# Kernel optimization log

Hardware: AMD Instinct MI355X
Metric: run time of the kernel (lower is better)

Reference implementation:

```python
import jax, jax.numpy as jnp
import numpy as np

B, L = 4, 2048
D_MODEL, D_INNER, D_STATE, DT_RANK, K = 512, 1024, 16, 64, 4


def setup_inputs() -> dict:
    key = jax.random.key(0)
    ks = jax.random.split(key, 21)
    def n(k, shape, s=0.02):
        return (jax.random.normal(k, shape) * s).astype(jnp.float32)
    inp = {"x": jax.random.normal(ks[0], (B, L, D_MODEL), jnp.float32)}
    for i, sfx in enumerate(("f", "b")):
        o = 1 + i * 8
        inp[f"W_in_{sfx}"] = n(ks[o], (2 * D_INNER, D_MODEL))
        inp[f"conv_w_{sfx}"] = n(ks[o + 1], (D_INNER, 1, K), 0.1)
        inp[f"conv_b_{sfx}"] = jnp.zeros((D_INNER,), jnp.float32)
        inp[f"A_log_{sfx}"] = (jax.random.normal(ks[o + 2], (D_STATE, D_INNER)) * 0.1).astype(jnp.float32)
        inp[f"D_{sfx}"] = jnp.ones((D_INNER,), jnp.float32)
        inp[f"Wx_{sfx}"] = n(ks[o + 3], (DT_RANK + 2 * D_STATE, D_INNER))
        inp[f"Wdt_{sfx}"] = n(ks[o + 4], (D_INNER, DT_RANK), DT_RANK ** -0.5)
        dt = jnp.exp(jax.random.uniform(ks[o + 5], (D_INNER,)) * (np.log(0.1) - np.log(0.001)) + np.log(0.001))
        inp[f"bdt_{sfx}"] = (dt + jnp.log(-jnp.expm1(-dt))).astype(jnp.float32)
        inp[f"Wout_{sfx}"] = n(ks[o + 6], (D_MODEL, D_INNER))
    return inp


def _mamba_block(x, W_in, conv_w, conv_b, A_log, Dp, Wx, Wdt, bdt, Wout):
    # x: [B, L, d_model]
    xz = jnp.einsum('bld,ed->ble', x, W_in)              # [B, L, 2*d_inner]
    xb, zb = xz[..., :D_INNER], xz[..., D_INNER:]
    # causal depthwise conv over time
    xc = jnp.transpose(xb, (0, 2, 1))                     # [B, M, L]
    xc = jax.lax.conv_general_dilated(
        xc, conv_w, window_strides=(1,), padding=[(K - 1, 0)],
        feature_group_count=D_INNER,
        dimension_numbers=('NCH', 'OIH', 'NCH')) + conv_b[None, :, None]
    xb = jax.nn.silu(jnp.transpose(xc, (0, 2, 1)))        # [B, L, M]
    # input-dependent SSM parameters
    proj = jnp.einsum('blm,pm->blp', xb, Wx)              # [B, L, dt_rank+2D]
    dt_in = proj[..., :DT_RANK]
    Bs = proj[..., DT_RANK:DT_RANK + D_STATE]             # [B, L, D]
    Cs = proj[..., DT_RANK + D_STATE:]                    # [B, L, D]
    dt = jax.nn.softplus(jnp.einsum('blr,mr->blm', dt_in, Wdt) + bdt)  # [B, L, M]
    A_T = -jnp.exp(A_log).T                               # [M, D]

    def step(h, inp):
        dt_t, x_t, B_t, C_t = inp                         # [B,M],[B,M],[B,D],[B,D]
        dA = jnp.exp(dt_t[:, :, None] * A_T[None])        # [B, M, D]
        h = dA * h + (dt_t * x_t)[:, :, None] * B_t[:, None, :]
        y_t = jnp.einsum('bmd,bd->bm', h, C_t)
        return h, y_t

    xs = (jnp.moveaxis(dt, 1, 0), jnp.moveaxis(xb, 1, 0),
          jnp.moveaxis(Bs, 1, 0), jnp.moveaxis(Cs, 1, 0))
    h0 = jnp.zeros((x.shape[0], D_INNER, D_STATE), x.dtype)
    _, ys = jax.lax.scan(step, h0, xs)                    # [L, B, M]
    y = jnp.moveaxis(ys, 0, 1) + Dp * xb                  # [B, L, M]
    y = y * jax.nn.silu(zb)                               # SiLU gate
    return jnp.einsum('blm,dm->bld', y, Wout)             # [B, L, d_model]


def reference(x,
              W_in_f, conv_w_f, conv_b_f, A_log_f, D_f, Wx_f, Wdt_f, bdt_f, Wout_f,
              W_in_b, conv_w_b, conv_b_b, A_log_b, D_b, Wx_b, Wdt_b, bdt_b, Wout_b):
    out_f = _mamba_block(x, W_in_f, conv_w_f, conv_b_f, A_log_f, D_f, Wx_f, Wdt_f, bdt_f, Wout_f)
    out_b = jnp.flip(_mamba_block(jnp.flip(x, 1), W_in_b, conv_w_b, conv_b_b, A_log_b, D_b, Wx_b, Wdt_b, bdt_b, Wout_b), 1)
    return out_f + out_b
```

## Files before the change

kernel.cpp:

```cpp
#include <hip/hip_runtime.h>
#include <hip/hip_bf16.h>
#include <cstdint>
#include <cstdio>

typedef float f32x4 __attribute__((ext_vector_type(4)));
typedef short s16x8 __attribute__((ext_vector_type(8)));

__device__ __forceinline__ float us2f(unsigned short u){
  union { unsigned int i; float f; } v; v.i = ((unsigned int)u) << 16; return v.f;
}
__device__ __forceinline__ unsigned short f2us(float f){
  union { float f; unsigned int i; } v; v.f = f;
  unsigned int r = v.i + 0x7fffu + ((v.i >> 16) & 1u);
  return (unsigned short)(r >> 16);
}
__device__ __forceinline__ s16x8 pack_bf8(f32x4 lo, f32x4 hi){
  s16x8 r;
  r[0]=(short)f2us(lo[0]); r[1]=(short)f2us(lo[1]); r[2]=(short)f2us(lo[2]); r[3]=(short)f2us(lo[3]);
  r[4]=(short)f2us(hi[0]); r[5]=(short)f2us(hi[1]); r[6]=(short)f2us(hi[2]); r[7]=(short)f2us(hi[3]);
  return r;
}

__global__ __launch_bounds__(256)
void prep_k(const float* __restrict__ x,
            const float* __restrict__ W_in_f, const float* __restrict__ W_in_b,
            const float* __restrict__ Wx_f,   const float* __restrict__ Wx_b,
            const float* __restrict__ Wdt_f,  const float* __restrict__ Wdt_b,
            const float* __restrict__ Wout_f, const float* __restrict__ Wout_b,
            const float* __restrict__ Alog_f, const float* __restrict__ Alog_b,
            const float* __restrict__ bdt_f,  const float* __restrict__ bdt_b,
            unsigned short* __restrict__ W1cat, unsigned short* __restrict__ Wxpad,
            unsigned short* __restrict__ Wdtb,  unsigned short* __restrict__ Woutcat,
            float* __restrict__ A2, float* __restrict__ bdtcat,
            unsigned short* __restrict__ xbf)
{
  long i = (long)blockIdx.x * 256 + threadIdx.x;
  if (i < 4194304) {
    xbf[i] = f2us(x[i]); return;
  }
  i -= 4194304;
  if (i < 2097152) {
    int n = (int)(i >> 9), k = (int)(i & 511);
    float v = (n < 2048) ? W_in_f[(long)n*512 + k] : W_in_b[(long)(n-2048)*512 + k];
    W1cat[i] = f2us(v); return;
  }
  i -= 2097152;
  if (i < 262144) {
    int dir = (int)(i >> 17); long r = i & 131071; int n = (int)(r >> 10), k = (int)(r & 1023);
    const float* Wx = dir ? Wx_b : Wx_f;
    Wxpad[(long)dir*131072 + r] = f2us(n < 96 ? Wx[(long)n*1024 + k] : 0.f); return;
  }
  i -= 262144;
  if (i < 131072) {
    int dir = (int)(i >> 16); long r = i & 65535;
    Wdtb[i] = f2us((dir ? Wdt_b : Wdt_f)[r]); return;
  }
  i -= 131072;
  if (i < 1048576) {
    int n = (int)(i >> 11), k = (int)(i & 2047);
    float v = (k < 1024) ? Wout_f[(long)n*1024 + k] : Wout_b[(long)n*1024 + (k-1024)];
    Woutcat[i] = f2us(v); return;
  }
  i -= 1048576;
  if (i < 32768) {
    int dir = (int)(i >> 14); long r = i & 16383; int m = (int)(r >> 4), d = (int)(r & 15);
    const float* Al = dir ? Alog_b : Alog_f;
    A2[i] = -__expf(Al[(long)d*1024 + m]) * 1.4426950408889634f; return;
  }
  i -= 32768;
  if (i < 2048) {
    int dir = (int)(i >> 10), m = (int)(i & 1023);
    bdtcat[i] = (dir ? bdt_b : bdt_f)[m]; return;
  }
}

template<int OUT_MODE, int A_IS_F32>
__global__ __launch_bounds__(256)
void gemm_bt(const void* __restrict__ Ap, const unsigned short* __restrict__ Bp,
             void* __restrict__ Cp, const float* __restrict__ biasp,
             int K, int lda, int ldb, int ldc,
             long az, long bz, long cz, int biasz)
{
  const int z   = blockIdx.z;
  const int tid = threadIdx.x;
  const int bm  = blockIdx.x, bn = blockIdx.y;

  __shared__ __align__(16) unsigned short Ash[128][32];
  __shared__ __align__(16) unsigned short Bsh[128][32];

  const int wave = tid >> 6, lane = tid & 63;
  const int wr = (wave >> 1) << 6, wc = (wave & 1) << 6;
  const int fr = lane & 15, fs = lane >> 4;

  const int r0 = tid >> 2, r1 = r0 + 64;
  const int sg = tid & 3,  kofs = sg << 3;

  const unsigned short* A16 = (const unsigned short*)Ap + (long)z * az;
  const float*          A32 = (const float*)Ap          + (long)z * az;
  const unsigned short* Bg  = Bp + (long)z * bz;

  const long aoff0 = (long)(bm*128 + r0)*lda + kofs;
  const long aoff1 = (long)(bm*128 + r1)*lda + kofs;
  const long boff0 = (long)(bn*128 + r0)*ldb + kofs;
  const long boff1 = (long)(bn*128 + r1)*ldb + kofs;

  f32x4 acc[4][4];
  #pragma unroll
  for (int i=0;i<4;i++)
    #pragma unroll
    for (int j=0;j<4;j++) acc[i][j] = (f32x4){0.f,0.f,0.f,0.f};

  s16x8 a0r{}, a1r{}, b0r{}, b1r{};
  f32x4 alo0{}, ahi0{}, alo1{}, ahi1{};

  if (A_IS_F32){
    alo0 = *(const f32x4*)(A32 + aoff0); ahi0 = *(const f32x4*)(A32 + aoff0 + 4);
    alo1 = *(const f32x4*)(A32 + aoff1); ahi1 = *(const f32x4*)(A32 + aoff1 + 4);
  } else {
    a0r = *(const s16x8*)(A16 + aoff0);
    a1r = *(const s16x8*)(A16 + aoff1);
  }
  b0r = *(const s16x8*)(Bg + boff0);
  b1r = *(const s16x8*)(Bg + boff1);

  const int NK  = K >> 5;
  const int sw0 = (sg ^ ((r0 >> 1) & 3)) << 3;
  const int sw1 = (sg ^ ((r1 >> 1) & 3)) << 3;

  for (int ks = 0; ks < NK; ++ks){
    __syncthreads();
    if (A_IS_F32){
      *(s16x8*)&Ash[r0][sw0] = pack_bf8(alo0, ahi0);
      *(s16x8*)&Ash[r1][sw1] = pack_bf8(alo1, ahi1);
    } else {
      *(s16x8*)&Ash[r0][sw0] = a0r;
      *(s16x8*)&Ash[r1][sw1] = a1r;
    }
    *(s16x8*)&Bsh[r0][sw0] = b0r;
    *(s16x8*)&Bsh[r1][sw1] = b1r;
    __syncthreads();
    if (ks + 1 < NK){
      const long k0 = (long)(ks + 1) << 5;
      if (A_IS_F32){
        alo0 = *(const f32x4*)(A32 + aoff0 + k0); ahi0 = *(const f32x4*)(A32 + aoff0 + k0 + 4);
        alo1 = *(const f32x4*)(A32 + aoff1 + k0); ahi1 = *(const f32x4*)(A32 + aoff1 + k0 + 4);
      } else {
        a0r = *(const s16x8*)(A16 + aoff0 + k0);
        a1r = *(const s16x8*)(A16 + aoff1 + k0);
      }
      b0r = *(const s16x8*)(Bg + boff0 + k0);
      b1r = *(const s16x8*)(Bg + boff1 + k0);
    }
    s16x8 af[4], bfv[4];
    #pragma unroll
    for (int i=0;i<4;i++){
      const int ar = wr + i*16 + fr;
      af[i]  = *(const s16x8*)&Ash[ar][(fs ^ ((ar >> 1) & 3)) << 3];
      const int br = wc + i*16 + fr;
      bfv[i] = *(const s16x8*)&Bsh[br][(fs ^ ((br >> 1) & 3)) << 3];
    }
    #pragma unroll
    for (int i=0;i<4;i++)
      #pragma unroll
      for (int j=0;j<4;j++)
        acc[i][j] = __builtin_amdgcn_mfma_f32_16x16x32_bf16(af[i], bfv[j], acc[i][j], 0, 0, 0);
  }

  #pragma unroll
  for (int i=0;i<4;i++){
    const int rowb = bm*128 + wr + i*16 + (fs << 2);
    #pragma unroll
    for (int j=0;j<4;j++){
      const int col = bn*128 + wc + j*16 + fr;
      #pragma unroll
      for (int e=0;e<4;e++){
        float v = acc[i][j][e];
        const long cidx = (long)z*cz + (long)(rowb + e)*ldc + col;
        if (OUT_MODE == 2){
          ((float*)Cp)[cidx] = v;
        } else if (OUT_MODE == 1){
          v += biasp[z*biasz + col];
          v = fmaxf(v, 0.f) + log1pf(__expf(-fabsf(v)));
          ((unsigned short*)Cp)[cidx] = f2us(v);
        } else {
          ((unsigned short*)Cp)[cidx] = f2us(v);
        }
      }
    }
  }
}

__global__ __launch_bounds__(256)
void conv_silu_k(const unsigned short* __restrict__ xz,
                 const float* __restrict__ wf, const float* __restrict__ cbf,
                 const float* __restrict__ wb, const float* __restrict__ cbb,
                 unsigned short* __restrict__ xbc)
{
  const long idx = (long)blockIdx.x * 256 + threadIdx.x;
  const int  col = (int)(idx & 2047);
  const long tok = idx >> 11;
  const int  dir = col >> 10, m = col & 1023;
  const int  l   = (int)(tok & 2047);
  const long rowb = tok << 12;
  const float* w  = dir ? wb : wf;
  float acc = dir ? cbb[m] : cbf[m];
  const int xcol = (dir << 11) + m;
  #pragma unroll
  for (int k=0;k<4;k++){
    const int pos = dir ? (l + 3 - k) : (l - 3 + k);
    if (pos >= 0 && pos < 2048)
      acc += w[m*4 + k] * us2f(xz[rowb + ((long)(pos - l) << 12) + xcol]);
  }
  const float s = acc / (1.f + __expf(-acc));
  xbc[idx] = f2us(s);
}

#define SCHUNK 64
#define NCHUNK 32

__global__ __launch_bounds__(256)
void scan1_k(const unsigned short* __restrict__ dtb, const unsigned short* __restrict__ xbc,
             const unsigned short* __restrict__ proj, const float* __restrict__ A2,
             float* __restrict__ hloc, float* __restrict__ Ssum)
{
  const int tidx = threadIdx.x;
  const int cb = blockIdx.x, c = blockIdx.y, bz = blockIdx.z;
  const int b = bz >> 1, dir = bz & 1;
  const int m = cb*256 + tidx;

  float a2[16];
  { const f32x4* p = (const f32x4*)(A2 + (((long)dir*1024 + m) << 4));
    f32x4 v0=p[0], v1=p[1], v2=p[2], v3=p[3];
    #pragma unroll
    for (int e=0;e<4;e++){ a2[e]=v0[e]; a2[4+e]=v1[e]; a2[8+e]=v2[e]; a2[12+e]=v3[e]; } }

  __shared__ float Bs[SCHUNK][16];
  if (tidx < 128){
    const int t = tidx >> 1, half = tidx & 1;
    const int l = dir ? (2047 - (c*SCHUNK + t)) : (c*SCHUNK + t);
    const long tok = (long)b*2048 + l;
    const s16x8 v = *(const s16x8*)(proj + (long)dir*1048576 + tok*128 + 64 + half*8);
    #pragma unroll
    for (int e=0;e<8;e++) Bs[t][half*8 + e] = us2f((unsigned short)v[e]);
  }
  __syncthreads();

  const int  l0 = dir ? (2047 - c*SCHUNK) : (c*SCHUNK);
  const int  ls = dir ? -1 : 1;
  const long tok0 = (long)b*2048 + l0;
  const unsigned short* dtp = dtb + (((long)dir) << 23) + tok0*1024 + m;
  const unsigned short* xvp = xbc + tok0*2048 + (dir << 10) + m;
  const long dstp = (long)ls*1024, xstp = (long)ls*2048;

  float h[16];
  #pragma unroll
  for (int d=0;d<16;d++) h[d]=0.f;
  float S = 0.f;

  unsigned short du = *dtp, xu = *xvp;
  for (int t=0;t<SCHUNK;t++){
    const float dt = us2f(du), xv = us2f(xu);
    dtp += dstp; xvp += xstp;
    du = *dtp; xu = *xvp;
    S += dt;
    const float u = dt * xv;
    const f32x4* bp = (const f32x4*)&Bs[t][0];
    f32x4 bv0=bp[0], bv1=bp[1], bv2=bp[2], bv3=bp[3];
    #pragma unroll
    for (int d=0;d<16;d++){
      const float bval = (d<4)? bv0[d&3] : (d<8)? bv1[d&3] : (d<12)? bv2[d&3] : bv3[d&3];
      const float a = __builtin_amdgcn_exp2f(dt * a2[d]);
      h[d] = __builtin_fmaf(a, h[d], u * bval);
    }
  }
  const long o = ((((long)bz * NCHUNK) + c)*1024 + m);
  f32x4* Hp = (f32x4*)(hloc + (o << 4));
  #pragma unroll
  for (int q=0;q<4;q++){
    f32x4 hv;
    #pragma unroll
    for (int e=0;e<4;e++) hv[e]=h[q*4+e];
    Hp[q]=hv;
  }
  Ssum[o] = S;
}

__global__ __launch_bounds__(256)
void scan2_k(const float* __restrict__ A2, const float* __restrict__ Ssum,
             float* __restrict__ hloc)
{
  const long idx = (long)blockIdx.x*256 + threadIdx.x;
  const long bz = idx >> 14; const int r = (int)(idx & 16383);
  const int dir = (int)(bz & 1);
  const float a2 = A2[((long)dir << 14) + r];
  const long base = bz * NCHUNK;
  float hs = 0.f;
  float hlN = hloc[base*16384 + r];
  float SN  = Ssum[base*1024 + (r >> 4)];
  for (int c=0;c<NCHUNK;c++){
    const float hl = hlN, Sv = SN;
    const int cn = (c+1 < NCHUNK) ? c+1 : c;
    hlN = hloc[(base+cn)*16384 + r];
    SN  = Ssum[(base+cn)*1024 + (r >> 4)];
    const float P = __builtin_amdgcn_exp2f(a2 * Sv);
    hloc[(base+c)*16384 + r] = hs;
    hs = __builtin_fmaf(P, hs, hl);
  }
}

__global__ __launch_bounds__(256)
void scan3_k(const unsigned short* __restrict__ dtb, const unsigned short* __restrict__ xbc,
             const unsigned short* __restrict__ proj, const float* __restrict__ A2,
             const float* __restrict__ hstart, const unsigned short* __restrict__ xz,
             const float* __restrict__ D_f, const float* __restrict__ D_b,
             unsigned short* __restrict__ ybuf)
{
  const int tidx = threadIdx.x;
  const int cb = blockIdx.x, c = blockIdx.y, bz = blockIdx.z;
  const int b = bz >> 1, dir = bz & 1;
  const int m = cb*256 + tidx;

  float a2[16];
  { const f32x4* p = (const f32x4*)(A2 + (((long)dir*1024 + m) << 4));
    f32x4 v0=p[0], v1=p[1], v2=p[2], v3=p[3];
    #pragma unroll
    for (int e=0;e<4;e++){ a2[e]=v0[e]; a2[4+e]=v1[e]; a2[8+e]=v2[e]; a2[12+e]=v3[e]; } }
  const float Dm = (dir ? D_b : D_f)[m];

  __shared__ float Bs[SCHUNK][16];
  __shared__ float Cs[SCHUNK][16];
  {
    const int half = tidx & 1;
    if (tidx < 128){
      const int t = tidx >> 1;
      const int l = dir ? (2047 - (c*SCHUNK + t)) : (c*SCHUNK + t);
      const long tok = (long)b*2048 + l;
      const s16x8 vb = *(const s16x8*)(proj + (long)dir*1048576 + tok*128 + 64 + half*8);
      #pragma unroll
      for (int e=0;e<8;e++) Bs[t][half*8+e] = us2f((unsigned short)vb[e]);
    } else {
      const int t = (tidx - 128) >> 1;
      const int l = dir ? (2047 - (c*SCHUNK + t)) : (c*SCHUNK + t);
      const long tok = (long)b*2048 + l;
      const s16x8 vc = *(const s16x8*)(proj + (long)dir*1048576 + tok*128 + 80 + half*8);
      #pragma unroll
      for (int e=0;e<8;e++) Cs[t][half*8+e] = us2f((unsigned short)vc[e]);
    }
  }

  float h[16];
  { const long o = ((((long)bz*NCHUNK) + c)*1024 + m) << 4;
    const f32x4* p = (const f32x4*)(hstart + o);
    f32x4 v0=p[0], v1=p[1], v2=p[2], v3=p[3];
    #pragma unroll
    for (int e=0;e<4;e++){ h[e]=v0[e]; h[4+e]=v1[e]; h[8+e]=v2[e]; h[12+e]=v3[e]; } }
  __syncthreads();

  const int  l0 = dir ? (2047 - c*SCHUNK) : (c*SCHUNK);
  const int  ls = dir ? -1 : 1;
  const long tok0 = (long)b*2048 + l0;
  const unsigned short* dtp = dtb + (((long)dir) << 23) + tok0*1024 + m;
  const unsigned short* xvp = xbc + tok0*2048 + (dir << 10) + m;
  const unsigned short* zp  = xz  + (tok0 << 12) + (dir << 11) + 1024 + m;
  unsigned short*       yp  = ybuf + tok0*2048 + (dir << 10) + m;
  const long dstp = (long)ls*1024, xstp = (long)ls*2048, zstp = (long)ls << 12;

  unsigned short du = *dtp, xu = *xvp, zu = *zp;
  for (int t=0;t<SCHUNK;t++){
    const float dt = us2f(du), xv = us2f(xu), zb = us2f(zu);
    dtp += dstp; xvp += xstp; zp += zstp;
    du = *dtp; xu = *xvp; zu = *zp;
    const float u = dt * xv;
    const f32x4* bp = (const f32x4*)&Bs[t][0];
    const f32x4* cp = (const f32x4*)&Cs[t][0];
    f32x4 bv0=bp[0], bv1=bp[1], bv2=bp[2], bv3=bp[3];
    f32x4 cv0=cp[0], cv1=cp[1], cv2=cp[2], cv3=cp[3];
    float y0=0.f, y1=0.f, y2=0.f, y3=0.f;
    #pragma unroll
    for (int d=0;d<16;d++){
      const float bval = (d<4)? bv0[d&3] : (d<8)? bv1[d&3] : (d<12)? bv2[d&3] : bv3[d&3];
      const float cval = (d<4)? cv0[d&3] : (d<8)? cv1[d&3] : (d<12)? cv2[d&3] : cv3[d&3];
      const float a = __builtin_amdgcn_exp2f(dt * a2[d]);
      h[d] = __builtin_fmaf(a, h[d], u * bval);
      if (d<4)       y0 = __builtin_fmaf(h[d], cval, y0);
      else if (d<8)  y1 = __builtin_fmaf(h[d], cval, y1);
      else if (d<12) y2 = __builtin_fmaf(h[d], cval, y2);
      else           y3 = __builtin_fmaf(h[d], cval, y3);
    }
    float y = ((y0+y1)+(y2+y3)) + Dm * xv;
    const float gate = zb / (1.f + __expf(-zb));
    *yp = f2us(y * gate);
    yp += xstp;
  }
}

extern "C" void kernel_launch(void* const* d_in, const int* in_sizes, int n_in,
                              void* d_out, int out_size, void* d_ws, size_t ws_size,
                              hipStream_t stream)
{
  const float* x      = (const float*)d_in[0];
  const float* W_in_f = (const float*)d_in[1];
  const float* convw_f= (const float*)d_in[2];
  const float* convb_f= (const float*)d_in[3];
  const float* Alog_f = (const float*)d_in[4];
  const float* D_f    = (const float*)d_in[5];
  const float* Wx_f   = (const float*)d_in[6];
  const float* Wdt_f  = (const float*)d_in[7];
  const float* bdt_f  = (const float*)d_in[8];
  const float* Wout_f = (const float*)d_in[9];
  const float* W_in_b = (const float*)d_in[10];
  const float* convw_b= (const float*)d_in[11];
  const float* convb_b= (const float*)d_in[12];
  const float* Alog_b = (const float*)d_in[13];
  const float* D_b    = (const float*)d_in[14];
  const float* Wx_b   = (const float*)d_in[15];
  const float* Wdt_b  = (const float*)d_in[16];
  const float* bdt_b  = (const float*)d_in[17];
  const float* Wout_b = (const float*)d_in[18];

  char* w = (char*)d_ws;
  auto carve = [&](size_t bytes) -> char* {
    char* p = w; w += (bytes + 255) & ~(size_t)255; return p;
  };
  unsigned short* W1cat   = (unsigned short*)carve(4096ULL*512*2);
  unsigned short* Wxpad   = (unsigned short*)carve(2ULL*128*1024*2);
  unsigned short* Wdtb    = (unsigned short*)carve(2ULL*1024*64*2);
  unsigned short* Woutcat = (unsigned short*)carve(512ULL*2048*2);
  float*          A2      = (float*)carve(2ULL*1024*16*4);
  float*          bdtcat  = (float*)carve(2048ULL*4);
  unsigned short* xz      = (unsigned short*)carve(8192ULL*4096*2);
  unsigned short* xbc     = (unsigned short*)carve(8192ULL*2048*2);
  unsigned short* proj    = (unsigned short*)carve(2ULL*8192*128*2);
  unsigned short* dtb     = (unsigned short*)carve(2ULL*8192*1024*2);
  unsigned short* ybuf    = (unsigned short*)carve(8192ULL*2048*2);
  float*          hloc    = (float*)carve(8ULL*NCHUNK*1024*16*4);
  float*          Ssum    = (float*)carve(8ULL*NCHUNK*1024*4);
  unsigned short* xbf     = ybuf;

  if ((size_t)(w - (char*)d_ws) > ws_size) {
    fprintf(stderr, "kernel_launch: ws too small (%zu needed, %zu given)\n",
            (size_t)(w - (char*)d_ws), ws_size);
    return;
  }

  prep_k<<<dim3(30344), 256, 0, stream>>>(x, W_in_f, W_in_b, Wx_f, Wx_b, Wdt_f, Wdt_b,
                                          Wout_f, Wout_b, Alog_f, Alog_b, bdt_f, bdt_b,
                                          W1cat, Wxpad, Wdtb, Woutcat, A2, bdtcat, xbf);
  gemm_bt<0,0><<<dim3(64,32,1), 256, 0, stream>>>(xbf, W1cat, xz, nullptr,
                                                  512, 512, 512, 4096, 0, 0, 0, 0);
  conv_silu_k<<<dim3(65536), 256, 0, stream>>>(xz, convw_f, convb_f, convw_b, convb_b, xbc);
  gemm_bt<0,0><<<dim3(64,1,2), 256, 0, stream>>>(xbc, Wxpad, proj, nullptr,
                                                 1024, 2048, 1024, 128,
                                                 1024, 131072, 1048576, 0);
  gemm_bt<1,0><<<dim3(64,8,2), 256, 0, stream>>>(proj, Wdtb, dtb, bdtcat,
                                                 64, 128, 64, 1024,
                                                 1048576, 65536, 8388608, 1024);
  scan1_k<<<dim3(4,NCHUNK,8), 256, 0, stream>>>(dtb, xbc, proj, A2, hloc, Ssum);
  scan2_k<<<dim3(512), 256, 0, stream>>>(A2, Ssum, hloc);
  scan3_k<<<dim3(4,NCHUNK,8), 256, 0, stream>>>(dtb, xbc, proj, A2, hloc, xz, D_f, D_b, ybuf);
  gemm_bt<2,0><<<dim3(64,4,1), 256, 0, stream>>>(ybuf, Woutcat, d_out, nullptr,
                                                 2048, 2048, 2048, 512, 0, 0, 0, 0);
}
```

Measured before the change: 355.8 us.

## Use direct global-to-LDS loads in GEMM and vectorize conv+SiLU kernel

The GEMM now stages A and B tiles through global_load_lds (direct global-to-LDS DMA), replacing the register-prefetch path and the XOR swizzle. It also drops the unused fp32-A variant. The conv_silu kernel now processes 8 channels per thread with 16-byte vector loads and stores instead of one scalar per thread. The trade-off is that the GEMM loses its software prefetch overlap, since loads and compute are serialized around the barriers. Dropping the swizzle may also bring back LDS bank conflicts on the fragment reads.

```diff
diff --git a/kernel.cpp b/kernel.cpp
--- a/kernel.cpp
+++ b/kernel.cpp
@@ -14,11 +14,10 @@
   unsigned int r = v.i + 0x7fffu + ((v.i >> 16) & 1u);
   return (unsigned short)(r >> 16);
 }
-__device__ __forceinline__ s16x8 pack_bf8(f32x4 lo, f32x4 hi){
-  s16x8 r;
-  r[0]=(short)f2us(lo[0]); r[1]=(short)f2us(lo[1]); r[2]=(short)f2us(lo[2]); r[3]=(short)f2us(lo[3]);
-  r[4]=(short)f2us(hi[0]); r[5]=(short)f2us(hi[1]); r[6]=(short)f2us(hi[2]); r[7]=(short)f2us(hi[3]);
-  return r;
+__device__ __forceinline__ void gload_lds16(const void* g, void* l){
+  __builtin_amdgcn_global_load_lds(
+      (const __attribute__((address_space(1))) unsigned int*)g,
+      (__attribute__((address_space(3))) unsigned int*)l, 16, 0, 0);
 }
 
 __global__ __launch_bounds__(256)
@@ -74,9 +73,9 @@
   }
 }
 
-template<int OUT_MODE, int A_IS_F32>
-__global__ __launch_bounds__(256)
-void gemm_bt(const void* __restrict__ Ap, const unsigned short* __restrict__ Bp,
+template<int OUT_MODE>
+__global__ __launch_bounds__(256)
+void gemm_bt(const unsigned short* __restrict__ Ap, const unsigned short* __restrict__ Bp,
              void* __restrict__ Cp, const float* __restrict__ biasp,
              int K, int lda, int ldb, int ldc,
              long az, long bz, long cz, int biasz)
@@ -92,17 +91,21 @@
   const int wr = (wave >> 1) << 6, wc = (wave & 1) << 6;
   const int fr = lane & 15, fs = lane >> 4;
 
-  const int r0 = tid >> 2, r1 = r0 + 64;
-  const int sg = tid & 3,  kofs = sg << 3;
-
-  const unsigned short* A16 = (const unsigned short*)Ap + (long)z * az;
-  const float*          A32 = (const float*)Ap          + (long)z * az;
-  const unsigned short* Bg  = Bp + (long)z * bz;
+  const int r0 = tid >> 2;
+  const int sg = tid & 3, kofs = sg << 3;
+
+  const unsigned short* Ag = Ap + (long)z * az;
+  const unsigned short* Bg = Bp + (long)z * bz;
 
   const long aoff0 = (long)(bm*128 + r0)*lda + kofs;
-  const long aoff1 = (long)(bm*128 + r1)*lda + kofs;
+  const long aoff1 = aoff0 + (long)64*lda;
   const long boff0 = (long)(bn*128 + r0)*ldb + kofs;
-  const long boff1 = (long)(bn*128 + r1)*ldb + kofs;
+  const long boff1 = boff0 + (long)64*ldb;
+
+  unsigned short* lA0 = &Ash[r0][kofs];
+  unsigned short* lA1 = &Ash[64 + r0][kofs];
+  unsigned short* lB0 = &Bsh[r0][kofs];
+  unsigned short* lB1 = &Bsh[64 + r0][kofs];
 
   f32x4 acc[4][4];
   #pragma unroll
@@ -110,54 +113,21 @@
     #pragma unroll
     for (int j=0;j<4;j++) acc[i][j] = (f32x4){0.f,0.f,0.f,0.f};
 
-  s16x8 a0r{}, a1r{}, b0r{}, b1r{};
-  f32x4 alo0{}, ahi0{}, alo1{}, ahi1{};
-
-  if (A_IS_F32){
-    alo0 = *(const f32x4*)(A32 + aoff0); ahi0 = *(const f32x4*)(A32 + aoff0 + 4);
-    alo1 = *(const f32x4*)(A32 + aoff1); ahi1 = *(const f32x4*)(A32 + aoff1 + 4);
-  } else {
-    a0r = *(const s16x8*)(A16 + aoff0);
-    a1r = *(const s16x8*)(A16 + aoff1);
-  }
-  b0r = *(const s16x8*)(Bg + boff0);
-  b1r = *(const s16x8*)(Bg + boff1);
-
-  const int NK  = K >> 5;
-  const int sw0 = (sg ^ ((r0 >> 1) & 3)) << 3;
-  const int sw1 = (sg ^ ((r1 >> 1) & 3)) << 3;
-
+  const int NK = K >> 5;
   for (int ks = 0; ks < NK; ++ks){
+    const long k0 = (long)ks << 5;
     __syncthreads();
-    if (A_IS_F32){
-      *(s16x8*)&Ash[r0][sw0] = pack_bf8(alo0, ahi0);
-      *(s16x8*)&Ash[r1][sw1] = pack_bf8(alo1, ahi1);
-    } else {
-      *(s16x8*)&Ash[r0][sw0] = a0r;
-      *(s16x8*)&Ash[r1][sw1] = a1r;
-    }
-    *(s16x8*)&Bsh[r0][sw0] = b0r;
-    *(s16x8*)&Bsh[r1][sw1] = b1r;
+    gload_lds16(Ag + aoff0 + k0, lA0);
+    gload_lds16(Ag + aoff1 + k0, lA1);
+    gload_lds16(Bg + boff0 + k0, lB0);
+    gload_lds16(Bg + boff1 + k0, lB1);
     __syncthreads();
-    if (ks + 1 < NK){
-      const long k0 = (long)(ks + 1) << 5;
-      if (A_IS_F32){
-        alo0 = *(const f32x4*)(A32 + aoff0 + k0); ahi0 = *(const f32x4*)(A32 + aoff0 + k0 + 4);
-        alo1 = *(const f32x4*)(A32 + aoff1 + k0); ahi1 = *(const f32x4*)(A32 + aoff1 + k0 + 4);
-      } else {
-        a0r = *(const s16x8*)(A16 + aoff0 + k0);
-        a1r = *(const s16x8*)(A16 + aoff1 + k0);
-      }
-      b0r = *(const s16x8*)(Bg + boff0 + k0);
-      b1r = *(const s16x8*)(Bg + boff1 + k0);
-    }
+
     s16x8 af[4], bfv[4];
     #pragma unroll
     for (int i=0;i<4;i++){
-      const int ar = wr + i*16 + fr;
-      af[i]  = *(const s16x8*)&Ash[ar][(fs ^ ((ar >> 1) & 3)) << 3];
-      const int br = wc + i*16 + fr;
-      bfv[i] = *(const s16x8*)&Bsh[br][(fs ^ ((br >> 1) & 3)) << 3];
+      af[i]  = *(const s16x8*)&Ash[wr + i*16 + fr][fs << 3];
+      bfv[i] = *(const s16x8*)&Bsh[wc + i*16 + fr][fs << 3];
     }
     #pragma unroll
     for (int i=0;i<4;i++)
@@ -196,23 +166,44 @@
                  const float* __restrict__ wb, const float* __restrict__ cbb,
                  unsigned short* __restrict__ xbc)
 {
-  const long idx = (long)blockIdx.x * 256 + threadIdx.x;
-  const int  col = (int)(idx & 2047);
-  const long tok = idx >> 11;
-  const int  dir = col >> 10, m = col & 1023;
-  const int  l   = (int)(tok & 2047);
+  const int tid = threadIdx.x;
+  const long tok = blockIdx.x;
+  const int l   = (int)(tok & 2047);
+  const int dir = tid >> 7;
+  const int mg  = (tid & 127) << 3;
+  const float* w  = dir ? wb  : wf;
+  const float* cb = dir ? cbb : cbf;
   const long rowb = tok << 12;
-  const float* w  = dir ? wb : wf;
-  float acc = dir ? cbb[m] : cbf[m];
-  const int xcol = (dir << 11) + m;
+  const int  xcol = (dir << 11) + mg;
+
+  f32x4 wv[8];
+  #pragma unroll
+  for (int e=0;e<8;e++) wv[e] = *(const f32x4*)(w + (mg + e)*4);
+  const f32x4 cb0 = *(const f32x4*)(cb + mg);
+  const f32x4 cb1 = *(const f32x4*)(cb + mg + 4);
+
+  float acc[8];
+  #pragma unroll
+  for (int e=0;e<4;e++){ acc[e]=cb0[e]; acc[4+e]=cb1[e]; }
+
   #pragma unroll
   for (int k=0;k<4;k++){
-    const int pos = dir ? (l + 3 - k) : (l - 3 + k);
-    if (pos >= 0 && pos < 2048)
-      acc += w[m*4 + k] * us2f(xz[rowb + ((long)(pos - l) << 12) + xcol]);
-  }
-  const float s = acc / (1.f + __expf(-acc));
-  xbc[idx] = f2us(s);
+    const int off = dir ? (3 - k) : (k - 3);
+    const int pos = l + off;
+    if (pos >= 0 && pos < 2048){
+      const s16x8 xv = *(const s16x8*)(xz + rowb + ((long)off << 12) + xcol);
+      #pragma unroll
+      for (int e=0;e<8;e++)
+        acc[e] = __builtin_fmaf(wv[e][k], us2f((unsigned short)xv[e]), acc[e]);
+    }
+  }
+  s16x8 out;
+  #pragma unroll
+  for (int e=0;e<8;e++){
+    const float s = acc[e] / (1.f + __expf(-acc[e]));
+    out[e] = (short)f2us(s);
+  }
+  *(s16x8*)(xbc + tok*2048 + (dir << 10) + mg) = out;
 }
 
 #define SCHUNK 64
@@ -446,18 +437,18 @@
   prep_k<<<dim3(30344), 256, 0, stream>>>(x, W_in_f, W_in_b, Wx_f, Wx_b, Wdt_f, Wdt_b,
                                           Wout_f, Wout_b, Alog_f, Alog_b, bdt_f, bdt_b,
                                           W1cat, Wxpad, Wdtb, Woutcat, A2, bdtcat, xbf);
-  gemm_bt<0,0><<<dim3(64,32,1), 256, 0, stream>>>(xbf, W1cat, xz, nullptr,
-                                                  512, 512, 512, 4096, 0, 0, 0, 0);
-  conv_silu_k<<<dim3(65536), 256, 0, stream>>>(xz, convw_f, convb_f, convw_b, convb_b, xbc);
-  gemm_bt<0,0><<<dim3(64,1,2), 256, 0, stream>>>(xbc, Wxpad, proj, nullptr,
-                                                 1024, 2048, 1024, 128,
-                                                 1024, 131072, 1048576, 0);
-  gemm_bt<1,0><<<dim3(64,8,2), 256, 0, stream>>>(proj, Wdtb, dtb, bdtcat,
-                                                 64, 128, 64, 1024,
-                                                 1048576, 65536, 8388608, 1024);
+  gemm_bt<0><<<dim3(64,32,1), 256, 0, stream>>>(xbf, W1cat, xz, nullptr,
+                                                512, 512, 512, 4096, 0, 0, 0, 0);
+  conv_silu_k<<<dim3(8192), 256, 0, stream>>>(xz, convw_f, convb_f, convw_b, convb_b, xbc);
+  gemm_bt<0><<<dim3(64,1,2), 256, 0, stream>>>(xbc, Wxpad, proj, nullptr,
+                                               1024, 2048, 1024, 128,
+                                               1024, 131072, 1048576, 0);
+  gemm_bt<1><<<dim3(64,8,2), 256, 0, stream>>>(proj, Wdtb, dtb, bdtcat,
+                                               64, 128, 64, 1024,
+                                               1048576, 65536, 8388608, 1024);
   scan1_k<<<dim3(4,NCHUNK,8), 256, 0, stream>>>(dtb, xbc, proj, A2, hloc, Ssum);
   scan2_k<<<dim3(512), 256, 0, stream>>>(A2, Ssum, hloc);
   scan3_k<<<dim3(4,NCHUNK,8), 256, 0, stream>>>(dtb, xbc, proj, A2, hloc, xz, D_f, D_b, ybuf);
-  gemm_bt<2,0><<<dim3(64,4,1), 256, 0, stream>>>(ybuf, Woutcat, d_out, nullptr,
-                                                 2048, 2048, 2048, 512, 0, 0, 0, 0);
-}
+  gemm_bt<2><<<dim3(64,4,1), 256, 0, stream>>>(ybuf, Woutcat, d_out, nullptr,
+                                               2048, 2048, 2048, 512, 0, 0, 0, 0);
+}
```

Result: faster. 347.8 us (-2.2%).
